# Optimization experiments

Hardware: AMD Instinct MI355X
Metric: run time of the kernel (lower is better)

The kernel has to match this reference:

```python
import jax, jax.numpy as jnp
import numpy as np

# --- MLA config (DeepSeek-V3 style, scaled) ---
HIDDEN = 4096
N_HEADS = 32
Q_LORA = 1536
KV_LORA = 512
ROPE_D = 64
NOPE_D = 128
V_D = 128
Q_HEAD_D = NOPE_D + ROPE_D  # 192
EPS = 1e-6
SCALING = Q_HEAD_D ** (-0.5)
ROPE_THETA = 10000.0
B, S = 1, 2048


def rms_norm(x, w):
    var = jnp.mean(jnp.square(x.astype(jnp.float32)), axis=-1, keepdims=True)
    return (x * jax.lax.rsqrt(var + EPS)).astype(x.dtype) * w


def rotate_half(x):
    x1, x2 = jnp.split(x, 2, axis=-1)
    return jnp.concatenate([-x2, x1], axis=-1)


def apply_rope(x, cos, sin):
    # x: [B, H, S, ROPE_D]; cos/sin: [B, S, ROPE_D] -> unsqueeze head dim
    c = cos[:, None, :, :]
    s = sin[:, None, :, :]
    return x * c + rotate_half(x) * s


def setup_inputs() -> dict:
    key = jax.random.key(0)
    ks = jax.random.split(key, 8)
    hidden_states = jax.random.normal(ks[0], (B, S, HIDDEN), dtype=jnp.float32)
    # real RoPE tables
    inv_freq = 1.0 / (ROPE_THETA ** (np.arange(0, ROPE_D, 2, dtype=np.float32) / ROPE_D))
    t = np.arange(S, dtype=np.float32)
    freqs = np.outer(t, inv_freq)                      # [S, ROPE_D/2]
    emb = np.concatenate([freqs, freqs], axis=-1)      # [S, ROPE_D]
    cos = jnp.asarray(np.cos(emb))[None].repeat(B, 0)  # [B, S, ROPE_D]
    sin = jnp.asarray(np.sin(emb))[None].repeat(B, 0)
    scale = lambda fan_in: 1.0 / np.sqrt(fan_in)
    w_q_a = jax.random.normal(ks[1], (Q_LORA, HIDDEN), dtype=jnp.float32) * scale(HIDDEN)
    q_a_ln_w = jnp.ones((Q_LORA,), dtype=jnp.float32)
    w_q_b = jax.random.normal(ks[2], (N_HEADS * Q_HEAD_D, Q_LORA), dtype=jnp.float32) * scale(Q_LORA)
    w_kv_a = jax.random.normal(ks[3], (KV_LORA + ROPE_D, HIDDEN), dtype=jnp.float32) * scale(HIDDEN)
    kv_a_ln_w = jnp.ones((KV_LORA,), dtype=jnp.float32)
    w_kv_b = jax.random.normal(ks[4], (N_HEADS * (NOPE_D + V_D), KV_LORA), dtype=jnp.float32) * scale(KV_LORA)
    w_o = jax.random.normal(ks[5], (HIDDEN, N_HEADS * V_D), dtype=jnp.float32) * scale(N_HEADS * V_D)
    return {
        'hidden_states': hidden_states, 'cos': cos, 'sin': sin,
        'w_q_a': w_q_a, 'q_a_ln_w': q_a_ln_w, 'w_q_b': w_q_b,
        'w_kv_a': w_kv_a, 'kv_a_ln_w': kv_a_ln_w, 'w_kv_b': w_kv_b, 'w_o': w_o,
    }


def reference(hidden_states, cos, sin, w_q_a, q_a_ln_w, w_q_b, w_kv_a, kv_a_ln_w, w_kv_b, w_o):
    b, s, _ = hidden_states.shape
    # --- Q path: low-rank down + RMSNorm + up ---
    q_lat = rms_norm(hidden_states @ w_q_a.T, q_a_ln_w)              # [B,S,Q_LORA]
    q = (q_lat @ w_q_b.T).reshape(b, s, N_HEADS, Q_HEAD_D)
    q = q.transpose(0, 2, 1, 3)                                       # [B,H,S,Q_HEAD_D]
    q_nope, q_rot = q[..., :NOPE_D], q[..., NOPE_D:]                  # (note: source names swapped)
    # --- KV path: shared compressed latent + single rotary key ---
    ckv = hidden_states @ w_kv_a.T                                    # [B,S,KV_LORA+ROPE_D]
    k_lat, k_rot = ckv[..., :KV_LORA], ckv[..., KV_LORA:]
    kv = (rms_norm(k_lat, kv_a_ln_w) @ w_kv_b.T).reshape(b, s, N_HEADS, NOPE_D + V_D)
    kv = kv.transpose(0, 2, 1, 3)                                     # [B,H,S,NOPE_D+V_D]
    k_nope, v = kv[..., :NOPE_D], kv[..., NOPE_D:]
    k_rot = k_rot.reshape(b, 1, s, ROPE_D)                            # single rotary key head
    # --- partial RoPE on rotary slices ---
    q_rot = apply_rope(q_rot, cos, sin)
    k_rot = apply_rope(k_rot, cos, sin)
    k_rot = jnp.broadcast_to(k_rot, (b, N_HEADS, s, ROPE_D))
    query = jnp.concatenate([q_rot, q_nope], axis=-1)                 # [B,H,S,192]
    key = jnp.concatenate([k_rot, k_nope], axis=-1)                   # [B,H,S,192]
    # --- eager causal attention ---
    scores = jnp.einsum('bhqd,bhkd->bhqk', query, key) * SCALING
    causal = jnp.tril(jnp.ones((s, s), dtype=bool))
    scores = jnp.where(causal[None, None], scores, jnp.finfo(scores.dtype).min)
    probs = jax.nn.softmax(scores, axis=-1)
    attn = jnp.einsum('bhqk,bhkd->bhqd', probs, v)                    # [B,H,S,V_D]
    attn = attn.transpose(0, 2, 1, 3).reshape(b, s, N_HEADS * V_D)
    return attn @ w_o.T                                               # [B,S,HIDDEN]
```

## Files before the change

kernel.cpp:

```cpp
#include <hip/hip_runtime.h>

typedef unsigned short u16;
typedef u16 u16x4 __attribute__((ext_vector_type(4)));
typedef u16 u16x8 __attribute__((ext_vector_type(8)));
typedef float f32x4 __attribute__((ext_vector_type(4)));
typedef __bf16 bf16x8 __attribute__((ext_vector_type(8)));

#define S_LEN 2048
#define HIDDEN_D 4096
#define NHEADS 32
#define QLORA 1536
#define KVLORA 512
#define ROPED 64
#define NOPED 128
#define VDIM 128
#define QHD 192
#define SCALING_F 0.07216878364870323f

__device__ __forceinline__ u16 f2bf(float x) {
  union { float f; unsigned u; } v; v.f = x;
  unsigned r = v.u + 0x7fffu + ((v.u >> 16) & 1u);
  return (u16)(r >> 16);
}

__device__ __forceinline__ f32x4 mfma_bf16(u16x8 a, u16x8 b, f32x4 c) {
  return __builtin_amdgcn_mfma_f32_16x16x32_bf16(
      __builtin_bit_cast(bf16x8, a), __builtin_bit_cast(bf16x8, b), c, 0, 0, 0);
}

__global__ __launch_bounds__(256) void cvt_kernel(const float* __restrict__ in,
                                                  u16* __restrict__ out, int n4) {
  int i = blockIdx.x * 256 + threadIdx.x;
  if (i >= n4) return;
  f32x4 v = ((const f32x4*)in)[i];
  u16x4 o;
  o[0] = f2bf(v[0]); o[1] = f2bf(v[1]); o[2] = f2bf(v[2]); o[3] = f2bf(v[3]);
  ((u16x4*)out)[i] = o;
}

__global__ __launch_bounds__(256, 2) void gemm_kernel(
    const u16* __restrict__ A, const float* __restrict__ B, float* __restrict__ C,
    int M, int N, int Ks, int lda, int ldb, int ldc)
{
  __shared__ u16 sA[2][128 * 64];
  __shared__ u16 sB[2][128 * 64];
  const int tid = threadIdx.x;
  const int wid = tid >> 6, lane = tid & 63;
  const int lr = lane & 15, lg = lane >> 4;
  const int nbn = (N + 127) >> 7;
  const int bx = blockIdx.x % nbn, by = blockIdx.x / nbn;
  const int bm = by << 7, bn = bx << 7;
  const int wm = (wid >> 1) << 6, wn = (wid & 1) << 6;
  const int kbase = blockIdx.y * Ks;
  C += (size_t)blockIdx.y * M * ldc;

  f32x4 acc[4][4] = {};
  u16x8 areg[4];
  f32x4 br0[4], br1[4];

  auto loadA = [&](int k0) {
#pragma unroll
    for (int i = 0; i < 4; ++i) {
      int chunk = i * 256 + tid;
      int row = chunk >> 3, c8 = chunk & 7;
      int gr = bm + row; if (gr >= M) gr = M - 1;
      areg[i] = *(const u16x8*)(A + (size_t)gr * lda + k0 + (c8 << 3));
    }
  };
  auto loadB = [&](int k0) {
#pragma unroll
    for (int i = 0; i < 4; ++i) {
      int chunk = i * 256 + tid;
      int n = chunk >> 3, c8 = chunk & 7;
      int gn = bn + n; if (gn >= N) gn = N - 1;
      const float* src = B + (size_t)gn * ldb + k0 + (c8 << 3);
      br0[i] = *(const f32x4*)src;
      br1[i] = *(const f32x4*)(src + 4);
    }
  };
  auto writeA = [&](int buf) {
#pragma unroll
    for (int i = 0; i < 4; ++i)
      *(u16x8*)&sA[buf][(i * 256 + tid) * 8] = areg[i];
  };
  auto writeB = [&](int buf) {
#pragma unroll
    for (int i = 0; i < 4; ++i) {
      u16x8 v;
      v[0] = f2bf(br0[i][0]); v[1] = f2bf(br0[i][1]);
      v[2] = f2bf(br0[i][2]); v[3] = f2bf(br0[i][3]);
      v[4] = f2bf(br1[i][0]); v[5] = f2bf(br1[i][1]);
      v[6] = f2bf(br1[i][2]); v[7] = f2bf(br1[i][3]);
      *(u16x8*)&sB[buf][(i * 256 + tid) * 8] = v;
    }
  };
  auto compute = [&](int buf) {
    const u16* pa = sA[buf];
    const u16* pb = sB[buf];
#pragma unroll
    for (int ks = 0; ks < 2; ++ks) {
      const int kof = ks * 32 + lg * 8;
      u16x8 av[4], bv[4];
#pragma unroll
      for (int m = 0; m < 4; ++m) av[m] = *(const u16x8*)&pa[(wm + m * 16 + lr) * 64 + kof];
#pragma unroll
      for (int n = 0; n < 4; ++n) bv[n] = *(const u16x8*)&pb[(wn + n * 16 + lr) * 64 + kof];
#pragma unroll
      for (int m = 0; m < 4; ++m)
#pragma unroll
        for (int n = 0; n < 4; ++n)
          acc[m][n] = mfma_bf16(av[m], bv[n], acc[m][n]);
    }
  };

  const int nk = Ks >> 6;
  loadA(kbase); loadB(kbase);
  writeA(0); writeB(0);
  __syncthreads();
  for (int t = 0; t < nk; ++t) {
    const int cur = t & 1;
    if (t + 1 < nk) { loadA(kbase + ((t + 1) << 6)); loadB(kbase + ((t + 1) << 6)); }
    compute(cur);
    if (t + 1 < nk) { writeA(cur ^ 1); writeB(cur ^ 1); }
    __syncthreads();
  }
#pragma unroll
  for (int m = 0; m < 4; ++m) {
    const int row0 = bm + wm + m * 16 + (lg << 2);
#pragma unroll
    for (int n = 0; n < 4; ++n) {
      const int col = bn + wn + n * 16 + lr;
      if (col < N) {
#pragma unroll
        for (int r = 0; r < 4; ++r)
          C[(size_t)(row0 + r) * ldc + col] = acc[m][n][r];
      }
    }
  }
}

__global__ __launch_bounds__(256) void rms_kernel(const float* __restrict__ X,
                                                  const float* __restrict__ w,
                                                  u16* __restrict__ out, int D,
                                                  int nparts, size_t pstride) {
  const int row = blockIdx.x;
  const float* x = X + (size_t)row * D;
  __shared__ float sb[4];
  float ss = 0.f;
  for (int i = threadIdx.x * 4; i < D; i += 1024) {
    f32x4 v = *(const f32x4*)&x[i];
    for (int pp = 1; pp < nparts; ++pp) {
      f32x4 v2 = *(const f32x4*)&x[pp * pstride + i];
      v[0] += v2[0]; v[1] += v2[1]; v[2] += v2[2]; v[3] += v2[3];
    }
    ss += v[0] * v[0] + v[1] * v[1] + v[2] * v[2] + v[3] * v[3];
  }
#pragma unroll
  for (int off = 32; off >= 1; off >>= 1) ss += __shfl_xor(ss, off, 64);
  if ((threadIdx.x & 63) == 0) sb[threadIdx.x >> 6] = ss;
  __syncthreads();
  const float inv = rsqrtf((sb[0] + sb[1] + sb[2] + sb[3]) / (float)D + 1e-6f);
  u16* o = out + (size_t)row * D;
  for (int i = threadIdx.x * 4; i < D; i += 1024) {
    f32x4 v = *(const f32x4*)&x[i];
    for (int pp = 1; pp < nparts; ++pp) {
      f32x4 v2 = *(const f32x4*)&x[pp * pstride + i];
      v[0] += v2[0]; v[1] += v2[1]; v[2] += v2[2]; v[3] += v2[3];
    }
    f32x4 wv = *(const f32x4*)&w[i];
    u16x4 u;
    u[0] = f2bf(v[0] * inv * wv[0]); u[1] = f2bf(v[1] * inv * wv[1]);
    u[2] = f2bf(v[2] * inv * wv[2]); u[3] = f2bf(v[3] * inv * wv[3]);
    *(u16x4*)&o[i] = u;
  }
}

__global__ __launch_bounds__(256) void ckv_epi_kernel(const float* __restrict__ ckv,
    const float* __restrict__ w, const float* __restrict__ cosp, const float* __restrict__ sinp,
    u16* __restrict__ klatn, u16* __restrict__ krot, int nparts, size_t pstride) {
  const int s = blockIdx.x;
  const float* x = ckv + (size_t)s * 576;
  __shared__ float sb[4];
  const int i2 = threadIdx.x * 2;
  float a = 0.f, b = 0.f;
  for (int pp = 0; pp < nparts; ++pp) {
    a += x[pp * pstride + i2];
    b += x[pp * pstride + i2 + 1];
  }
  float ss = a * a + b * b;
#pragma unroll
  for (int off = 32; off >= 1; off >>= 1) ss += __shfl_xor(ss, off, 64);
  if ((threadIdx.x & 63) == 0) sb[threadIdx.x >> 6] = ss;
  __syncthreads();
  const float inv = rsqrtf((sb[0] + sb[1] + sb[2] + sb[3]) / 512.0f + 1e-6f);
  klatn[(size_t)s * 512 + i2]     = f2bf(a * inv * w[i2]);
  klatn[(size_t)s * 512 + i2 + 1] = f2bf(b * inv * w[i2 + 1]);
  if (threadIdx.x < 64) {
    const int d = threadIdx.x;
    float xr = 0.f, rrabs = 0.f;
    for (int pp = 0; pp < nparts; ++pp) {
      xr += x[pp * pstride + 512 + d];
      rrabs += x[pp * pstride + 512 + ((d < 32) ? (d + 32) : (d - 32))];
    }
    const float rr = (d < 32) ? -rrabs : rrabs;
    krot[(size_t)s * 64 + d] = f2bf(xr * cosp[s * 64 + d] + rr * sinp[s * 64 + d]);
  }
}

__global__ __launch_bounds__(256) void q_epi_kernel(const float* __restrict__ q_raw,
    const float* __restrict__ cosp, const float* __restrict__ sinp, u16* __restrict__ Qb) {
  const int s = blockIdx.x;
  const float* x = q_raw + (size_t)s * 6144;
  for (int idx = threadIdx.x; idx < 6144; idx += 256) {
    const int h = idx / 192, d = idx - h * 192;
    float v;
    if (d < 64) {
      const float xr = x[h * 192 + 128 + d];
      const float rr = (d < 32) ? -x[h * 192 + 160 + d] : x[h * 192 + 96 + d];
      v = xr * cosp[s * 64 + d] + rr * sinp[s * 64 + d];
    } else {
      v = x[h * 192 + d - 64];
    }
    Qb[((size_t)h * 2048 + s) * QHD + d] = f2bf(v * SCALING_F);
  }
}

__global__ __launch_bounds__(256) void kv_epi_kernel(const float* __restrict__ kv_raw,
    u16* __restrict__ Knope, u16* __restrict__ Vt) {
  const int h = blockIdx.x & 31, st = blockIdx.x >> 5;
  const int s0 = st << 6;
  __shared__ u16 tile[64][VDIM + 2];
  for (int i = 0; i < 32; ++i) {
    const int idx = i * 256 + threadIdx.x;
    const int r = idx >> 7, d = idx & 127;
    const float kn = kv_raw[(size_t)(s0 + r) * 8192 + h * 256 + d];
    Knope[((size_t)h * 2048 + s0 + r) * 128 + d] = f2bf(kn);
    tile[r][d] = f2bf(kv_raw[(size_t)(s0 + r) * 8192 + h * 256 + 128 + d]);
  }
  __syncthreads();
  for (int i = 0; i < 32; ++i) {
    const int idx = i * 256 + threadIdx.x;
    const int d = idx >> 6, r = idx & 63;
    Vt[((size_t)h * 128 + d) * 2048 + s0 + r] = tile[r][d];
  }
}

__global__ __launch_bounds__(256, 2) void flash_kernel(
    const u16* __restrict__ Qb, const u16* __restrict__ Krot,
    const u16* __restrict__ Knope, const u16* __restrict__ Vt,
    u16* __restrict__ attnb)
{
  const int h = blockIdx.x & 31, qt = blockIdx.x >> 5;
  const int q0 = qt << 7;
  __shared__ u16 sK[64][QHD];
  __shared__ u16 sV[VDIM][64];
  __shared__ u16 sP[4][32][64];
  const int tid = threadIdx.x;
  const int wid = tid >> 6, lane = tid & 63;
  const int lr = lane & 15, lg = lane >> 4;

  u16x8 qf[2][6];
#pragma unroll
  for (int m = 0; m < 2; ++m) {
    const int row = q0 + wid * 32 + m * 16 + lr;
#pragma unroll
    for (int kk = 0; kk < 6; ++kk)
      qf[m][kk] = *(const u16x8*)&Qb[((size_t)h * 2048 + row) * QHD + kk * 32 + lg * 8];
  }

  f32x4 acc[2][8] = {};
  float mx[2][4], ls[2][4];
#pragma unroll
  for (int m = 0; m < 2; ++m)
#pragma unroll
    for (int r = 0; r < 4; ++r) { mx[m][r] = -1e30f; ls[m][r] = 0.f; }

  const int nkv = q0 + 128;
  u16x8 kreg[6], vreg[4];

  auto loadKV = [&](int kv0) {
#pragma unroll
    for (int i = 0; i < 6; ++i) {
      const int chunk = i * 256 + tid;
      const int row = chunk / 24, cc = chunk % 24;
      const u16* src = (cc < 8)
          ? &Krot[(size_t)(kv0 + row) * 64 + cc * 8]
          : &Knope[((size_t)h * 2048 + kv0 + row) * 128 + (cc - 8) * 8];
      kreg[i] = *(const u16x8*)src;
    }
#pragma unroll
    for (int i = 0; i < 4; ++i) {
      const int chunk = i * 256 + tid;
      const int d = chunk >> 3, c = chunk & 7;
      vreg[i] = *(const u16x8*)&Vt[((size_t)h * VDIM + d) * 2048 + kv0 + c * 8];
    }
  };

  loadKV(0);
  for (int kv0 = 0; kv0 < nkv; kv0 += 64) {
    __syncthreads();
    u16* kbase = &sK[0][0];
#pragma unroll
    for (int i = 0; i < 6; ++i) *(u16x8*)&kbase[(size_t)(i * 256 + tid) * 8] = kreg[i];
    u16* vbase = &sV[0][0];
#pragma unroll
    for (int i = 0; i < 4; ++i) *(u16x8*)&vbase[(size_t)(i * 256 + tid) * 8] = vreg[i];
    __syncthreads();
    if (kv0 + 64 < nkv) loadKV(kv0 + 64);

    f32x4 sc[2][4] = {};
#pragma unroll
    for (int kk = 0; kk < 6; ++kk) {
      u16x8 bfr[4];
#pragma unroll
      for (int n = 0; n < 4; ++n) bfr[n] = *(const u16x8*)&sK[n * 16 + lr][kk * 32 + lg * 8];
#pragma unroll
      for (int m = 0; m < 2; ++m)
#pragma unroll
        for (int n = 0; n < 4; ++n)
          sc[m][n] = mfma_bf16(qf[m][kk], bfr[n], sc[m][n]);
    }

    if (kv0 + 63 > q0 + wid * 32) {
#pragma unroll
      for (int m = 0; m < 2; ++m)
#pragma unroll
        for (int n = 0; n < 4; ++n) {
          const int kv = kv0 + n * 16 + lr;
#pragma unroll
          for (int r = 0; r < 4; ++r) {
            const int rowq = q0 + wid * 32 + m * 16 + lg * 4 + r;
            if (kv > rowq) sc[m][n][r] = -1e30f;
          }
        }
    }

#pragma unroll
    for (int m = 0; m < 2; ++m) {
      float rs[4];
#pragma unroll
      for (int r = 0; r < 4; ++r) {
        float v = fmaxf(fmaxf(sc[m][0][r], sc[m][1][r]), fmaxf(sc[m][2][r], sc[m][3][r]));
#pragma unroll
        for (int off = 1; off < 16; off <<= 1) v = fmaxf(v, __shfl_xor(v, off, 64));
        const float mnew = fmaxf(mx[m][r], v);
        const float alpha = __expf(mx[m][r] - mnew);
        mx[m][r] = mnew;
        ls[m][r] *= alpha;
#pragma unroll
        for (int df = 0; df < 8; ++df) acc[m][df][r] *= alpha;
        rs[r] = 0.f;
      }
#pragma unroll
      for (int n = 0; n < 4; ++n)
#pragma unroll
        for (int r = 0; r < 4; ++r) {
          const float p = __expf(sc[m][n][r] - mx[m][r]);
          rs[r] += p;
          sP[wid][m * 16 + lg * 4 + r][n * 16 + lr] = f2bf(p);
        }
#pragma unroll
      for (int r = 0; r < 4; ++r) {
        float v = rs[r];
#pragma unroll
        for (int off = 1; off < 16; off <<= 1) v += __shfl_xor(v, off, 64);
        ls[m][r] += v;
      }
    }

#pragma unroll
    for (int ks = 0; ks < 2; ++ks) {
      u16x8 pf0 = *(const u16x8*)&sP[wid][lr][ks * 32 + lg * 8];
      u16x8 pf1 = *(const u16x8*)&sP[wid][16 + lr][ks * 32 + lg * 8];
#pragma unroll
      for (int df = 0; df < 8; ++df) {
        u16x8 vf = *(const u16x8*)&sV[df * 16 + lr][ks * 32 + lg * 8];
        acc[0][df] = mfma_bf16(pf0, vf, acc[0][df]);
        acc[1][df] = mfma_bf16(pf1, vf, acc[1][df]);
      }
    }
  }

#pragma unroll
  for (int m = 0; m < 2; ++m)
#pragma unroll
    for (int df = 0; df < 8; ++df) {
      const int col = h * 128 + df * 16 + lr;
#pragma unroll
      for (int r = 0; r < 4; ++r) {
        const int row = q0 + wid * 32 + m * 16 + lg * 4 + r;
        attnb[(size_t)row * 4096 + col] = f2bf(acc[m][df][r] / ls[m][r]);
      }
    }
}

extern "C" void kernel_launch(void* const* d_in, const int* in_sizes, int n_in,
                              void* d_out, int out_size, void* d_ws, size_t ws_size,
                              hipStream_t stream) {
  (void)in_sizes; (void)n_in; (void)out_size; (void)ws_size;
  const float* hidden  = (const float*)d_in[0];
  const float* cosp    = (const float*)d_in[1];
  const float* sinp    = (const float*)d_in[2];
  const float* w_q_a   = (const float*)d_in[3];
  const float* q_a_ln  = (const float*)d_in[4];
  const float* w_q_b   = (const float*)d_in[5];
  const float* w_kv_a  = (const float*)d_in[6];
  const float* kv_a_ln = (const float*)d_in[7];
  const float* w_kv_b  = (const float*)d_in[8];
  const float* w_o     = (const float*)d_in[9];
  float* out = (float*)d_out;

  char* p = (char*)d_ws;
  auto alloc = [&](size_t bytes) { char* r = p; p += (bytes + 255) & ~(size_t)255; return r; };
  u16* Hb    = (u16*)alloc((size_t)S_LEN * HIDDEN_D * 2);
  u16* qlatn = (u16*)alloc((size_t)S_LEN * QLORA * 2);
  u16* klatn = (u16*)alloc((size_t)S_LEN * KVLORA * 2);
  u16* krot  = (u16*)alloc((size_t)S_LEN * ROPED * 2);
  u16* Qb    = (u16*)alloc((size_t)NHEADS * S_LEN * QHD * 2);
  u16* Knope = (u16*)alloc((size_t)NHEADS * S_LEN * NOPED * 2);
  u16* Vt    = (u16*)alloc((size_t)NHEADS * VDIM * S_LEN * 2);
  u16* attnb = (u16*)alloc((size_t)S_LEN * 4096 * 2);
  float* qa_part  = (float*)alloc((size_t)2 * S_LEN * QLORA * 4);
  float* kva_part = (float*)alloc((size_t)4 * S_LEN * 576 * 4);
  float* raw = (float*)alloc((size_t)S_LEN * 8192 * 4);
  float* q_raw  = raw;
  float* kv_raw = raw;

  cvt_kernel<<<(S_LEN * HIDDEN_D / 4 + 255) / 256, 256, 0, stream>>>(hidden, Hb, S_LEN * HIDDEN_D / 4);
  gemm_kernel<<<dim3(16 * 12, 2), 256, 0, stream>>>(Hb, w_q_a, qa_part, 2048, 1536, 2048, 4096, 4096, 1536);
  gemm_kernel<<<dim3(16 * 5, 4), 256, 0, stream>>>(Hb, w_kv_a, kva_part, 2048, 576, 1024, 4096, 4096, 576);
  rms_kernel<<<2048, 256, 0, stream>>>(qa_part, q_a_ln, qlatn, 1536, 2, (size_t)S_LEN * QLORA);
  ckv_epi_kernel<<<2048, 256, 0, stream>>>(kva_part, kv_a_ln, cosp, sinp, klatn, krot, 4, (size_t)S_LEN * 576);
  gemm_kernel<<<dim3(16 * 48, 1), 256, 0, stream>>>(qlatn, w_q_b, q_raw, 2048, 6144, 1536, 1536, 1536, 6144);
  q_epi_kernel<<<2048, 256, 0, stream>>>(q_raw, cosp, sinp, Qb);
  gemm_kernel<<<dim3(16 * 64, 1), 256, 0, stream>>>(klatn, w_kv_b, kv_raw, 2048, 8192, 512, 512, 512, 8192);
  kv_epi_kernel<<<1024, 256, 0, stream>>>(kv_raw, Knope, Vt);
  flash_kernel<<<512, 256, 0, stream>>>(Qb, krot, Knope, Vt, attnb);
  gemm_kernel<<<dim3(16 * 32, 1), 256, 0, stream>>>(attnb, w_o, out, 2048, 4096, 4096, 4096, 4096, 4096);
}
```

Measured before the change: 628.7 us.

## Pre-convert weights to bf16, fuse KV-b epilogue into GEMM, bf16 q_raw

Weights are converted to bf16 once per call by separate cvt kernels, so the GEMMs load bf16 B tiles directly instead of converting fp32 inside the k-loop. The KV-b GEMM now writes Knope and transposed Vt straight from its epilogue, which removes kv_epi_kernel and the fp32 kv_raw round trip. The Q-b GEMM stores bf16 output for q_epi. The cost is five extra conversion launches that read and write about 60M weight elements on every call, plus an extra rounding of q before RoPE.

```diff
diff --git a/kernel.cpp b/kernel.cpp
--- a/kernel.cpp
+++ b/kernel.cpp
@@ -22,6 +22,9 @@
   unsigned r = v.u + 0x7fffu + ((v.u >> 16) & 1u);
   return (u16)(r >> 16);
 }
+__device__ __forceinline__ float bf2f(u16 x) {
+  union { unsigned u; float f; } v; v.u = ((unsigned)x) << 16; return v.f;
+}
 
 __device__ __forceinline__ f32x4 mfma_bf16(u16x8 a, u16x8 b, f32x4 c) {
   return __builtin_amdgcn_mfma_f32_16x16x32_bf16(
@@ -38,92 +41,81 @@
   ((u16x4*)out)[i] = o;
 }
 
-__global__ __launch_bounds__(256, 2) void gemm_kernel(
-    const u16* __restrict__ A, const float* __restrict__ B, float* __restrict__ C,
+
+#define GEMM_PROLOGUE()                                                        \
+  __shared__ u16 sA[2][128 * 64];                                              \
+  __shared__ u16 sB[2][128 * 64];                                              \
+  const int tid = threadIdx.x;                                                 \
+  const int wid = tid >> 6, lane = tid & 63;                                   \
+  const int lr = lane & 15, lg = lane >> 4;                                    \
+  const int nbn = (N + 127) >> 7;                                              \
+  const int bx = blockIdx.x % nbn, by = blockIdx.x / nbn;                      \
+  const int bm = by << 7, bn = bx << 7;                                        \
+  const int wm = (wid >> 1) << 6, wn = (wid & 1) << 6;                         \
+  const int kbase = blockIdx.y * Ks;                                           \
+  f32x4 acc[4][4] = {};                                                        \
+  u16x8 areg[4], breg[4];                                                      \
+  auto loadA = [&](int k0) {                                                   \
+    _Pragma("unroll")                                                          \
+    for (int i = 0; i < 4; ++i) {                                              \
+      int chunk = i * 256 + tid;                                               \
+      int row = chunk >> 3, c8 = chunk & 7;                                    \
+      int gr = bm + row; if (gr >= M) gr = M - 1;                              \
+      areg[i] = *(const u16x8*)(A + (size_t)gr * lda + k0 + (c8 << 3));        \
+    }                                                                          \
+  };                                                                           \
+  auto loadB = [&](int k0) {                                                   \
+    _Pragma("unroll")                                                          \
+    for (int i = 0; i < 4; ++i) {                                              \
+      int chunk = i * 256 + tid;                                               \
+      int n = chunk >> 3, c8 = chunk & 7;                                      \
+      int gn = bn + n; if (gn >= N) gn = N - 1;                                \
+      breg[i] = *(const u16x8*)(B + (size_t)gn * ldb + k0 + (c8 << 3));        \
+    }                                                                          \
+  };                                                                           \
+  auto writeAB = [&](int buf) {                                                \
+    _Pragma("unroll")                                                          \
+    for (int i = 0; i < 4; ++i) {                                              \
+      *(u16x8*)&sA[buf][(i * 256 + tid) * 8] = areg[i];                        \
+      *(u16x8*)&sB[buf][(i * 256 + tid) * 8] = breg[i];                        \
+    }                                                                          \
+  };                                                                           \
+  auto compute = [&](int buf) {                                                \
+    const u16* pa = sA[buf];                                                   \
+    const u16* pb = sB[buf];                                                   \
+    _Pragma("unroll")                                                          \
+    for (int ks = 0; ks < 2; ++ks) {                                           \
+      const int kof = ks * 32 + lg * 8;                                        \
+      u16x8 av[4], bv[4];                                                      \
+      _Pragma("unroll")                                                        \
+      for (int m = 0; m < 4; ++m) av[m] = *(const u16x8*)&pa[(wm + m * 16 + lr) * 64 + kof]; \
+      _Pragma("unroll")                                                        \
+      for (int n = 0; n < 4; ++n) bv[n] = *(const u16x8*)&pb[(wn + n * 16 + lr) * 64 + kof]; \
+      _Pragma("unroll")                                                        \
+      for (int m = 0; m < 4; ++m)                                              \
+        _Pragma("unroll")                                                      \
+        for (int n = 0; n < 4; ++n)                                            \
+          acc[m][n] = mfma_bf16(av[m], bv[n], acc[m][n]);                      \
+    }                                                                          \
+  };                                                                           \
+  const int nk = Ks >> 6;                                                      \
+  loadA(kbase); loadB(kbase);                                                  \
+  writeAB(0);                                                                  \
+  __syncthreads();                                                             \
+  for (int t = 0; t < nk; ++t) {                                               \
+    const int cur = t & 1;                                                     \
+    if (t + 1 < nk) { loadA(kbase + ((t + 1) << 6)); loadB(kbase + ((t + 1) << 6)); } \
+    compute(cur);                                                              \
+    if (t + 1 < nk) { writeAB(cur ^ 1); }                                      \
+    __syncthreads();                                                           \
+  }
+
+__global__ __launch_bounds__(256, 2) void gemm_ff(
+    const u16* __restrict__ A, const u16* __restrict__ B, float* __restrict__ C,
     int M, int N, int Ks, int lda, int ldb, int ldc)
 {
-  __shared__ u16 sA[2][128 * 64];
-  __shared__ u16 sB[2][128 * 64];
-  const int tid = threadIdx.x;
-  const int wid = tid >> 6, lane = tid & 63;
-  const int lr = lane & 15, lg = lane >> 4;
-  const int nbn = (N + 127) >> 7;
-  const int bx = blockIdx.x % nbn, by = blockIdx.x / nbn;
-  const int bm = by << 7, bn = bx << 7;
-  const int wm = (wid >> 1) << 6, wn = (wid & 1) << 6;
-  const int kbase = blockIdx.y * Ks;
   C += (size_t)blockIdx.y * M * ldc;
-
-  f32x4 acc[4][4] = {};
-  u16x8 areg[4];
-  f32x4 br0[4], br1[4];
-
-  auto loadA = [&](int k0) {
-#pragma unroll
-    for (int i = 0; i < 4; ++i) {
-      int chunk = i * 256 + tid;
-      int row = chunk >> 3, c8 = chunk & 7;
-      int gr = bm + row; if (gr >= M) gr = M - 1;
-      areg[i] = *(const u16x8*)(A + (size_t)gr * lda + k0 + (c8 << 3));
-    }
-  };
-  auto loadB = [&](int k0) {
-#pragma unroll
-    for (int i = 0; i < 4; ++i) {
-      int chunk = i * 256 + tid;
-      int n = chunk >> 3, c8 = chunk & 7;
-      int gn = bn + n; if (gn >= N) gn = N - 1;
-      const float* src = B + (size_t)gn * ldb + k0 + (c8 << 3);
-      br0[i] = *(const f32x4*)src;
-      br1[i] = *(const f32x4*)(src + 4);
-    }
-  };
-  auto writeA = [&](int buf) {
-#pragma unroll
-    for (int i = 0; i < 4; ++i)
-      *(u16x8*)&sA[buf][(i * 256 + tid) * 8] = areg[i];
-  };
-  auto writeB = [&](int buf) {
-#pragma unroll
-    for (int i = 0; i < 4; ++i) {
-      u16x8 v;
-      v[0] = f2bf(br0[i][0]); v[1] = f2bf(br0[i][1]);
-      v[2] = f2bf(br0[i][2]); v[3] = f2bf(br0[i][3]);
-      v[4] = f2bf(br1[i][0]); v[5] = f2bf(br1[i][1]);
-      v[6] = f2bf(br1[i][2]); v[7] = f2bf(br1[i][3]);
-      *(u16x8*)&sB[buf][(i * 256 + tid) * 8] = v;
-    }
-  };
-  auto compute = [&](int buf) {
-    const u16* pa = sA[buf];
-    const u16* pb = sB[buf];
-#pragma unroll
-    for (int ks = 0; ks < 2; ++ks) {
-      const int kof = ks * 32 + lg * 8;
-      u16x8 av[4], bv[4];
-#pragma unroll
-      for (int m = 0; m < 4; ++m) av[m] = *(const u16x8*)&pa[(wm + m * 16 + lr) * 64 + kof];
-#pragma unroll
-      for (int n = 0; n < 4; ++n) bv[n] = *(const u16x8*)&pb[(wn + n * 16 + lr) * 64 + kof];
-#pragma unroll
-      for (int m = 0; m < 4; ++m)
-#pragma unroll
-        for (int n = 0; n < 4; ++n)
-          acc[m][n] = mfma_bf16(av[m], bv[n], acc[m][n]);
-    }
-  };
-
-  const int nk = Ks >> 6;
-  loadA(kbase); loadB(kbase);
-  writeA(0); writeB(0);
-  __syncthreads();
-  for (int t = 0; t < nk; ++t) {
-    const int cur = t & 1;
-    if (t + 1 < nk) { loadA(kbase + ((t + 1) << 6)); loadB(kbase + ((t + 1) << 6)); }
-    compute(cur);
-    if (t + 1 < nk) { writeA(cur ^ 1); writeB(cur ^ 1); }
-    __syncthreads();
-  }
+  GEMM_PROLOGUE()
 #pragma unroll
   for (int m = 0; m < 4; ++m) {
     const int row0 = bm + wm + m * 16 + (lg << 2);
@@ -134,6 +126,51 @@
 #pragma unroll
         for (int r = 0; r < 4; ++r)
           C[(size_t)(row0 + r) * ldc + col] = acc[m][n][r];
+      }
+    }
+  }
+}
+
+__global__ __launch_bounds__(256, 2) void gemm_fb(
+    const u16* __restrict__ A, const u16* __restrict__ B, u16* __restrict__ C,
+    int M, int N, int Ks, int lda, int ldb, int ldc)
+{
+  GEMM_PROLOGUE()
+#pragma unroll
+  for (int m = 0; m < 4; ++m) {
+    const int row0 = bm + wm + m * 16 + (lg << 2);
+#pragma unroll
+    for (int n = 0; n < 4; ++n) {
+      const int col = bn + wn + n * 16 + lr;
+#pragma unroll
+      for (int r = 0; r < 4; ++r)
+        C[(size_t)(row0 + r) * ldc + col] = f2bf(acc[m][n][r]);
+    }
+  }
+}
+
+__global__ __launch_bounds__(256, 2) void gemm_kvb(
+    const u16* __restrict__ A, const u16* __restrict__ B,
+    u16* __restrict__ Knope, u16* __restrict__ Vt,
+    int M, int N, int Ks, int lda, int ldb)
+{
+  GEMM_PROLOGUE()
+#pragma unroll
+  for (int m = 0; m < 4; ++m) {
+    const int row0 = bm + wm + m * 16 + (lg << 2);
+#pragma unroll
+    for (int n = 0; n < 4; ++n) {
+      const int col = bn + wn + n * 16 + lr;
+      const int h = col >> 8, c = col & 255;
+      if (c < 128) {
+#pragma unroll
+        for (int r = 0; r < 4; ++r)
+          Knope[((size_t)h * 2048 + row0 + r) * 128 + c] = f2bf(acc[m][n][r]);
+      } else {
+        u16x4 v;
+        v[0] = f2bf(acc[m][n][0]); v[1] = f2bf(acc[m][n][1]);
+        v[2] = f2bf(acc[m][n][2]); v[3] = f2bf(acc[m][n][3]);
+        *(u16x4*)&Vt[((size_t)h * 128 + (c - 128)) * 2048 + row0] = v;
       }
     }
   }
@@ -207,41 +244,21 @@
   }
 }
 
-__global__ __launch_bounds__(256) void q_epi_kernel(const float* __restrict__ q_raw,
+__global__ __launch_bounds__(256) void q_epi_kernel(const u16* __restrict__ q_raw,
     const float* __restrict__ cosp, const float* __restrict__ sinp, u16* __restrict__ Qb) {
   const int s = blockIdx.x;
-  const float* x = q_raw + (size_t)s * 6144;
+  const u16* x = q_raw + (size_t)s * 6144;
   for (int idx = threadIdx.x; idx < 6144; idx += 256) {
     const int h = idx / 192, d = idx - h * 192;
     float v;
     if (d < 64) {
-      const float xr = x[h * 192 + 128 + d];
-      const float rr = (d < 32) ? -x[h * 192 + 160 + d] : x[h * 192 + 96 + d];
+      const float xr = bf2f(x[h * 192 + 128 + d]);
+      const float rr = (d < 32) ? -bf2f(x[h * 192 + 160 + d]) : bf2f(x[h * 192 + 96 + d]);
       v = xr * cosp[s * 64 + d] + rr * sinp[s * 64 + d];
     } else {
-      v = x[h * 192 + d - 64];
+      v = bf2f(x[h * 192 + d - 64]);
     }
     Qb[((size_t)h * 2048 + s) * QHD + d] = f2bf(v * SCALING_F);
-  }
-}
-
-__global__ __launch_bounds__(256) void kv_epi_kernel(const float* __restrict__ kv_raw,
-    u16* __restrict__ Knope, u16* __restrict__ Vt) {
-  const int h = blockIdx.x & 31, st = blockIdx.x >> 5;
-  const int s0 = st << 6;
-  __shared__ u16 tile[64][VDIM + 2];
-  for (int i = 0; i < 32; ++i) {
-    const int idx = i * 256 + threadIdx.x;
-    const int r = idx >> 7, d = idx & 127;
-    const float kn = kv_raw[(size_t)(s0 + r) * 8192 + h * 256 + d];
-    Knope[((size_t)h * 2048 + s0 + r) * 128 + d] = f2bf(kn);
-    tile[r][d] = f2bf(kv_raw[(size_t)(s0 + r) * 8192 + h * 256 + 128 + d]);
-  }
-  __syncthreads();
-  for (int i = 0; i < 32; ++i) {
-    const int idx = i * 256 + threadIdx.x;
-    const int d = idx >> 6, r = idx & 63;
-    Vt[((size_t)h * 128 + d) * 2048 + s0 + r] = tile[r][d];
   }
 }
 
@@ -412,29 +429,37 @@
 
   char* p = (char*)d_ws;
   auto alloc = [&](size_t bytes) { char* r = p; p += (bytes + 255) & ~(size_t)255; return r; };
-  u16* Hb    = (u16*)alloc((size_t)S_LEN * HIDDEN_D * 2);
-  u16* qlatn = (u16*)alloc((size_t)S_LEN * QLORA * 2);
-  u16* klatn = (u16*)alloc((size_t)S_LEN * KVLORA * 2);
-  u16* krot  = (u16*)alloc((size_t)S_LEN * ROPED * 2);
-  u16* Qb    = (u16*)alloc((size_t)NHEADS * S_LEN * QHD * 2);
-  u16* Knope = (u16*)alloc((size_t)NHEADS * S_LEN * NOPED * 2);
-  u16* Vt    = (u16*)alloc((size_t)NHEADS * VDIM * S_LEN * 2);
-  u16* attnb = (u16*)alloc((size_t)S_LEN * 4096 * 2);
+  u16* Hb     = (u16*)alloc((size_t)S_LEN * HIDDEN_D * 2);
+  u16* qlatn  = (u16*)alloc((size_t)S_LEN * QLORA * 2);
+  u16* klatn  = (u16*)alloc((size_t)S_LEN * KVLORA * 2);
+  u16* krot   = (u16*)alloc((size_t)S_LEN * ROPED * 2);
+  u16* Qb     = (u16*)alloc((size_t)NHEADS * S_LEN * QHD * 2);
+  u16* Knope  = (u16*)alloc((size_t)NHEADS * S_LEN * NOPED * 2);
+  u16* Vt     = (u16*)alloc((size_t)NHEADS * VDIM * S_LEN * 2);
+  u16* attnb  = (u16*)alloc((size_t)S_LEN * 4096 * 2);
+  u16* Wqa    = (u16*)alloc((size_t)QLORA * HIDDEN_D * 2);
+  u16* Wqb    = (u16*)alloc((size_t)6144 * QLORA * 2);
+  u16* Wkva   = (u16*)alloc((size_t)576 * HIDDEN_D * 2);
+  u16* Wkvb   = (u16*)alloc((size_t)8192 * KVLORA * 2);
+  u16* Wo     = (u16*)alloc((size_t)HIDDEN_D * 4096 * 2);
+  u16* qraw16 = (u16*)alloc((size_t)S_LEN * 6144 * 2);
   float* qa_part  = (float*)alloc((size_t)2 * S_LEN * QLORA * 4);
   float* kva_part = (float*)alloc((size_t)4 * S_LEN * 576 * 4);
-  float* raw = (float*)alloc((size_t)S_LEN * 8192 * 4);
-  float* q_raw  = raw;
-  float* kv_raw = raw;
 
   cvt_kernel<<<(S_LEN * HIDDEN_D / 4 + 255) / 256, 256, 0, stream>>>(hidden, Hb, S_LEN * HIDDEN_D / 4);
-  gemm_kernel<<<dim3(16 * 12, 2), 256, 0, stream>>>(Hb, w_q_a, qa_part, 2048, 1536, 2048, 4096, 4096, 1536);
-  gemm_kernel<<<dim3(16 * 5, 4), 256, 0, stream>>>(Hb, w_kv_a, kva_part, 2048, 576, 1024, 4096, 4096, 576);
+  cvt_kernel<<<(QLORA * HIDDEN_D / 4 + 255) / 256, 256, 0, stream>>>(w_q_a, Wqa, QLORA * HIDDEN_D / 4);
+  cvt_kernel<<<(6144 * QLORA / 4 + 255) / 256, 256, 0, stream>>>(w_q_b, Wqb, 6144 * QLORA / 4);
+  cvt_kernel<<<(576 * HIDDEN_D / 4 + 255) / 256, 256, 0, stream>>>(w_kv_a, Wkva, 576 * HIDDEN_D / 4);
+  cvt_kernel<<<(8192 * KVLORA / 4 + 255) / 256, 256, 0, stream>>>(w_kv_b, Wkvb, 8192 * KVLORA / 4);
+  cvt_kernel<<<(HIDDEN_D * 4096 / 4 + 255) / 256, 256, 0, stream>>>(w_o, Wo, HIDDEN_D * 4096 / 4);
+
+  gemm_ff<<<dim3(16 * 12, 2), 256, 0, stream>>>(Hb, Wqa, qa_part, 2048, 1536, 2048, 4096, 4096, 1536);
+  gemm_ff<<<dim3(16 * 5, 4), 256, 0, stream>>>(Hb, Wkva, kva_part, 2048, 576, 1024, 4096, 4096, 576);
   rms_kernel<<<2048, 256, 0, stream>>>(qa_part, q_a_ln, qlatn, 1536, 2, (size_t)S_LEN * QLORA);
   ckv_epi_kernel<<<2048, 256, 0, stream>>>(kva_part, kv_a_ln, cosp, sinp, klatn, krot, 4, (size_t)S_LEN * 576);
-  gemm_kernel<<<dim3(16 * 48, 1), 256, 0, stream>>>(qlatn, w_q_b, q_raw, 2048, 6144, 1536, 1536, 1536, 6144);
-  q_epi_kernel<<<2048, 256, 0, stream>>>(q_raw, cosp, sinp, Qb);
-  gemm_kernel<<<dim3(16 * 64, 1), 256, 0, stream>>>(klatn, w_kv_b, kv_raw, 2048, 8192, 512, 512, 512, 8192);
-  kv_epi_kernel<<<1024, 256, 0, stream>>>(kv_raw, Knope, Vt);
+  gemm_fb<<<dim3(16 * 48, 1), 256, 0, stream>>>(qlatn, Wqb, qraw16, 2048, 6144, 1536, 1536, 1536, 6144);
+  q_epi_kernel<<<2048, 256, 0, stream>>>(qraw16, cosp, sinp, Qb);
+  gemm_kvb<<<dim3(16 * 64, 1), 256, 0, stream>>>(klatn, Wkvb, Knope, Vt, 2048, 8192, 512, 512, 512);
   flash_kernel<<<512, 256, 0, stream>>>(Qb, krot, Knope, Vt, attnb);
-  gemm_kernel<<<dim3(16 * 32, 1), 256, 0, stream>>>(attnb, w_o, out, 2048, 4096, 4096, 4096, 4096, 4096);
-}
+  gemm_ff<<<dim3(16 * 32, 1), 256, 0, stream>>>(attnb, Wo, out, 2048, 4096, 4096, 4096, 4096, 4096);
+}
```

After: 604.7 us. 1.04x faster.
